# Optimization experiments

Hardware: AMD Instinct MI355X
Metric: run time of the kernel (lower is better)

The kernel has to match this reference:

```python
import jax, jax.numpy as jnp
import numpy as np

WINDOW = 25
DIM_HEAD = 32


def _rel_pos_indices(w):
    # replicates the torch buffer: grid of (i,j) positions, pairwise offsets
    pos = np.arange(w)
    gi, gj = np.meshgrid(pos, pos, indexing='ij')
    grid = np.stack([gi.reshape(-1), gj.reshape(-1)], axis=-1)  # (w*w, 2)
    rel = grid[:, None, :] - grid[None, :, :] + (w - 1)          # (n, n, 2)
    return jnp.asarray(rel[..., 0] * (2 * w - 1) + rel[..., 1], dtype=jnp.int32)


def setup_inputs() -> dict:
    key = jax.random.key(0)
    k1, k2, k3, k4 = jax.random.split(key, 4)
    b, d, w = 32, 256, WINDOW
    heads = d // DIM_HEAD
    x = jax.random.normal(k1, (b, d, w, w), dtype=jnp.float32)
    W_qkv = jax.random.normal(k2, (d, 3 * d), dtype=jnp.float32) * 0.02
    W_out = jax.random.normal(k3, (d, d), dtype=jnp.float32) * 0.02
    rel_emb = jax.random.normal(k4, ((2 * w - 1) ** 2, heads), dtype=jnp.float32) * 0.02
    return {"x": x, "W_qkv": W_qkv, "W_out": W_out, "rel_emb": rel_emb}


def reference(x, W_qkv, W_out, rel_emb):
    b, d, H, W = x.shape
    h = d // DIM_HEAD
    scale = DIM_HEAD ** -0.5
    n = H * W

    # b d H W -> b n d
    xf = x.reshape(b, d, n).transpose(0, 2, 1)
    qkv = xf @ W_qkv                       # (b, n, 3d); columns ordered q,k,v
    q, k, v = jnp.split(qkv, 3, axis=-1)

    def to_heads(t):
        return t.reshape(b, n, h, DIM_HEAD).transpose(0, 2, 1, 3)  # b h n dh

    q = to_heads(q) * scale
    k = to_heads(k)
    v = to_heads(v)

    sim = jnp.einsum('bhid,bhjd->bhij', q, k)          # (b, h, n, n)
    bias = rel_emb[_rel_pos_indices(H)]                # (n, n, h)
    sim = sim + bias.transpose(2, 0, 1)[None]          # add per-head bias
    attn = jax.nn.softmax(sim, axis=-1)

    out = jnp.einsum('bhij,bhjd->bhid', attn, v)       # (b, h, n, dh)
    # b m (H W) dh -> b H W (m dh)  (head-major channel concat)
    out = out.transpose(0, 2, 1, 3).reshape(b, H, W, d)
    out = out @ W_out                                  # output projection (no bias)
    return out.transpose(0, 3, 1, 2)                   # b d H W
```

## Files before the change

kernel.cpp:

```cpp
#include <hip/hip_runtime.h>
#include <hip/hip_bf16.h>
#include <cstdint>

typedef __bf16 bf16x8 __attribute__((ext_vector_type(8)));
typedef __bf16 bf16x4 __attribute__((ext_vector_type(4)));
typedef float  f32x4  __attribute__((ext_vector_type(4)));

__device__ __forceinline__ int div25(int v) { return (v * 1311) >> 15; }

#if __has_builtin(__builtin_amdgcn_exp2f)
__device__ __forceinline__ float fast_exp2(float x) { return __builtin_amdgcn_exp2f(x); }
#else
__device__ __forceinline__ float fast_exp2(float x) { return exp2f(x); }
#endif

__device__ __forceinline__ int sniff_isbf(const void* p)
{
    const unsigned short* x = (const unsigned short*)p;
    int cnt = 0;
    #pragma unroll
    for (int i = 0; i < 16; ++i) {
        int e = (x[2 * i] >> 7) & 0xFF;
        cnt += (e >= 90 && e <= 143) ? 1 : 0;
    }
    return cnt > 8;
}

__global__ void k_transcvt(const void* __restrict__ src, __bf16* __restrict__ dst,
                           int R, int C, int Cpad, int src_bstride, int dst_bstride)
{
    __shared__ float tile[64][65];
    int isbf = sniff_isbf(src);
    int b  = blockIdx.z;
    int r0 = blockIdx.y * 64, c0 = blockIdx.x * 64;
    int tc = threadIdx.x & 63, tg = threadIdx.x >> 6;
    const unsigned short* sb = (const unsigned short*)src + (size_t)b * src_bstride;
    const float*          sf = (const float*)src          + (size_t)b * src_bstride;
    #pragma unroll
    for (int rr = 0; rr < 16; ++rr) {
        int r = r0 + tg * 16 + rr, c = c0 + tc;
        float v = 0.f;
        if (r < R && c < C) {
            if (isbf) v = __uint_as_float((unsigned int)sb[r * C + c] << 16);
            else      v = sf[r * C + c];
        }
        tile[tg * 16 + rr][tc] = v;
    }
    __syncthreads();
    __bf16* d = dst + (size_t)b * dst_bstride;
    #pragma unroll
    for (int rr = 0; rr < 16; ++rr) {
        int c = c0 + tg * 16 + rr, r = r0 + tc;
        if (c < Cpad && r < R) d[(size_t)c * R + r] = (__bf16)tile[tc][tg * 16 + rr];
    }
}

__global__ void k_wprep(const void* __restrict__ Wqkv, const void* __restrict__ Wout,
                        __bf16* __restrict__ Wt, __bf16* __restrict__ WoT)
{
    __shared__ float tile[64][65];
    int isbf = sniff_isbf(Wqkv);
    int isqkv = (blockIdx.x < 12);
    int bx = isqkv ? blockIdx.x : (blockIdx.x - 12);
    const void* src = isqkv ? Wqkv : Wout;
    __bf16* dst = isqkv ? Wt : WoT;
    int R = 256, C = isqkv ? 768 : 256;
    int r0 = blockIdx.y * 64, c0 = bx * 64;
    int tc = threadIdx.x & 63, tg = threadIdx.x >> 6;
    const unsigned short* sb = (const unsigned short*)src;
    const float*          sf = (const float*)src;
    #pragma unroll
    for (int rr = 0; rr < 16; ++rr) {
        int r = r0 + tg * 16 + rr, c = c0 + tc;
        float v;
        if (isbf) v = __uint_as_float((unsigned int)sb[r * C + c] << 16);
        else      v = sf[r * C + c];
        tile[tg * 16 + rr][tc] = v;
    }
    __syncthreads();
    const float qs = 0.25503494f;
    #pragma unroll
    for (int rr = 0; rr < 16; ++rr) {
        int c = c0 + tg * 16 + rr, r = r0 + tc;
        float v = tile[tc][tg * 16 + rr];
        if (isqkv && c < 256) v *= qs;
        dst[(size_t)c * R + r] = (__bf16)v;
    }
}

__global__ void k_bias(const void* __restrict__ rel, __bf16* __restrict__ biasC)
{
    const float LOG2E = 1.4426950408889634f;
    int isbf = sniff_isbf(rel);
    int ig = blockIdx.x;
    int h  = blockIdx.y;
    for (int t0 = 0; t0 < 10; ++t0) {
        int t  = t0 * 256 + threadIdx.x;
        int jc = t >> 7;
        int js = (t >> 6) & 1;
        int ln = t & 63;
        int q = ln >> 4, l = ln & 15;
        int i = ig * 16 + l;
        int di = div25(i), ri = i - 25 * di;
        bf16x4 out;
        #pragma unroll
        for (int rr = 0; rr < 4; ++rr) {
            int j = jc * 32 + js * 16 + q * 4 + rr;
            float v;
            if (j >= 625) {
                v = -43281.f;
            } else {
                int dj = div25(j);
                int idx = (di - dj + 24) * 49 + ri - (j - 25 * dj) + 24;
                idx = min(max(idx, 0), 2400);
                float r;
                if (isbf) r = (float)((const __bf16*)rel)[idx * 8 + h];
                else      r = ((const float*)rel)[idx * 8 + h];
                v = r * LOG2E;
            }
            out[rr] = (__bf16)v;
        }
        *(bf16x4*)(biasC + ((size_t)(h * 40 + ig) * 20 + jc) * 512 + js * 256 + ln * 4) = out;
    }
}

#define AS(r, c) pool[(size_t)(r) * 40 + (c)]
#define BS(r, c) pool[5120 + (size_t)(r) * 40 + (c)]
#define CS(r, c) pool[(size_t)(r) * 44 + (c)]
__global__ __launch_bounds__(256, 2) void k_qkv(
    const __bf16* __restrict__ xT,
    const __bf16* __restrict__ Wt,
    __bf16* __restrict__ Q,
    __bf16* __restrict__ Km,
    __bf16* __restrict__ Vt)
{
    __shared__ __align__(16) __bf16 pool[10240];
    int b = blockIdx.z, pt = blockIdx.y, jt = blockIdx.x;
    int p0 = pt * 128, j0 = jt * 128;
    int tid = threadIdx.x;
    int w = tid >> 6, lane = tid & 63;
    int quad = lane >> 4, l15 = lane & 15;
    int wr = w >> 1, wc = w & 1;

    int srow = tid >> 2, scg = (tid & 3) * 8;
    const __bf16* ag  = xT + ((size_t)(b * 640 + p0 + srow) * 256) + scg;
    const __bf16* ag2 = ag + 64 * 256;
    const __bf16* bg  = Wt + ((size_t)(j0 + srow) * 256) + scg;
    const __bf16* bg2 = bg + 64 * 256;

    f32x4 acc[4][4] = {};
    for (int kk = 0; kk < 8; ++kk) {
        int c0 = kk * 32;
        bf16x8 a0 = *(const bf16x8*)(ag + c0);
        bf16x8 a1 = *(const bf16x8*)(ag2 + c0);
        bf16x8 b0 = *(const bf16x8*)(bg + c0);
        bf16x8 b1 = *(const bf16x8*)(bg2 + c0);
        __syncthreads();
        *(bf16x8*)(&AS(srow, scg))      = a0;
        *(bf16x8*)(&AS(64 + srow, scg)) = a1;
        *(bf16x8*)(&BS(srow, scg))      = b0;
        *(bf16x8*)(&BS(64 + srow, scg)) = b1;
        __syncthreads();
        bf16x8 af[4], bfr[4];
        #pragma unroll
        for (int t = 0; t < 4; ++t) {
            af[t]  = *(const bf16x8*)(&AS(wr * 64 + t * 16 + l15, quad * 8));
            bfr[t] = *(const bf16x8*)(&BS(wc * 64 + t * 16 + l15, quad * 8));
        }
        #pragma unroll
        for (int i = 0; i < 4; ++i)
            #pragma unroll
            for (int j = 0; j < 4; ++j)
                acc[i][j] = __builtin_amdgcn_mfma_f32_16x16x32_bf16(af[i], bfr[j], acc[i][j], 0, 0, 0);
    }

    if (jt < 4) {
        for (int r = 0; r < 4; ++r) {
            __syncthreads();
            if (wc == (r >> 1)) {
                #pragma unroll
                for (int i = 0; i < 4; ++i) {
                    #pragma unroll
                    for (int js = 0; js < 2; ++js) {
                        int jp = (r & 1) * 2 + js;
                        int col = js * 16 + l15;
                        int prow = wr * 64 + i * 16 + quad * 4;
                        #pragma unroll
                        for (int rr = 0; rr < 4; ++rr)
                            CS(prow + rr, col) = (__bf16)acc[i][jp][rr];
                    }
                }
            }
            __syncthreads();
            int jj = j0 + r * 32;
            __bf16* dst; int hh;
            if (jj < 256) { hh = jj >> 5; dst = Q; }
            else          { hh = (jj - 256) >> 5; dst = Km; }
            int p = tid >> 1, d0 = (tid & 1) * 16;
            size_t base = ((size_t)((b * 8 + hh) * 640) + p0 + p) * 32 + d0;
            #pragma unroll
            for (int k4 = 0; k4 < 4; ++k4) {
                bf16x4 v4 = *(const bf16x4*)(&CS(p, d0 + k4 * 4));
                *(bf16x4*)(dst + base + k4 * 4) = v4;
            }
        }
    } else {
        #pragma unroll
        for (int i = 0; i < 4; ++i) {
            #pragma unroll
            for (int j = 0; j < 4; ++j) {
                int jj = j0 + wc * 64 + j * 16 + l15 - 512;
                int h = jj >> 5, t = jj & 31;
                int p = p0 + wr * 64 + i * 16 + quad * 4;
                bf16x4 vv;
                #pragma unroll
                for (int rr = 0; rr < 4; ++rr) vv[rr] = (__bf16)acc[i][j][rr];
                *(bf16x4*)(Vt + ((size_t)((b * 8 + h) * 32) + t) * 640 + p) = vv;
            }
        }
    }
}

__global__ __launch_bounds__(128, 3) void k_attn(
    const __bf16* __restrict__ Q,
    const __bf16* __restrict__ Km,
    const __bf16* __restrict__ Vt,
    const __bf16* __restrict__ biasC,
    __bf16* __restrict__ ctx)
{
    __shared__ __align__(16) __bf16 P[2][2][64][40];
    __shared__ float ssum[2][64];
    int bh = blockIdx.x, b = bh >> 3, h = bh & 7;
    int tid = threadIdx.x, w = tid >> 6, lane = tid & 63;
    int quad = lane >> 4, l15 = lane & 15;
    int i0 = (blockIdx.y * 2 + w) * 64;

    bf16x8 qa[4];
    #pragma unroll
    for (int m = 0; m < 4; ++m)
        qa[m] = *(const bf16x8*)(Q + ((size_t)bh * 640 + i0 + 16 * m + l15) * 32 + quad * 8);
    const __bf16* kbase = Km + (size_t)bh * 640 * 32 + quad * 8;
    const __bf16* vbase = Vt + ((size_t)bh * 32 + l15) * 640 + quad * 8;
    const __bf16* bcb   = biasC + (size_t)(h * 40 + (i0 >> 4)) * 10240 + lane * 4;

    f32x4 o[4][2] = {};
    float psum[4] = {0.f, 0.f, 0.f, 0.f};

    bf16x8 k0 = *(const bf16x8*)(kbase + (size_t)l15 * 32);
    bf16x8 k1 = *(const bf16x8*)(kbase + (size_t)(16 + l15) * 32);
    bf16x4 bc[4][2];
    #pragma unroll
    for (int m = 0; m < 4; ++m) {
        bc[m][0] = *(const bf16x4*)(bcb + m * 10240);
        bc[m][1] = *(const bf16x4*)(bcb + m * 10240 + 256);
    }
    bf16x8 vC0 = {}, vC1 = {};

    for (int c = 0; c < 20; ++c) {
        int buf = c & 1;
        if (c > 0) {
            #pragma unroll
            for (int m = 0; m < 4; ++m) {
                bf16x8 pa = *(const bf16x8*)(&P[w][buf ^ 1][16 * m + l15][quad * 8]);
                o[m][0] = __builtin_amdgcn_mfma_f32_16x16x32_bf16(pa, vC0, o[m][0], 0, 0, 0);
                o[m][1] = __builtin_amdgcn_mfma_f32_16x16x32_bf16(pa, vC1, o[m][1], 0, 0, 0);
            }
        }
        int cn = min(c + 1, 19);
        bf16x8 k0n = *(const bf16x8*)(kbase + (size_t)(cn * 32 + l15) * 32);
        bf16x8 k1n = *(const bf16x8*)(kbase + (size_t)(cn * 32 + 16 + l15) * 32);
        bf16x8 vN0 = *(const bf16x8*)(vbase + c * 32);
        bf16x8 vN1 = *(const bf16x8*)(vbase + (size_t)16 * 640 + c * 32);
        bf16x4 bn[4][2];
        #pragma unroll
        for (int m = 0; m < 4; ++m) {
            bn[m][0] = *(const bf16x4*)(bcb + m * 10240 + cn * 512);
            bn[m][1] = *(const bf16x4*)(bcb + m * 10240 + cn * 512 + 256);
        }
        #pragma unroll
        for (int m = 0; m < 4; ++m) {
            f32x4 f0, f1;
            #pragma unroll
            for (int rr = 0; rr < 4; ++rr) { f0[rr] = (float)bc[m][0][rr]; f1[rr] = (float)bc[m][1][rr]; }
            f32x4 s0 = __builtin_amdgcn_mfma_f32_16x16x32_bf16(k0, qa[m], f0, 0, 0, 0);
            f32x4 s1 = __builtin_amdgcn_mfma_f32_16x16x32_bf16(k1, qa[m], f1, 0, 0, 0);
            bf16x4 p0, p1;
            #pragma unroll
            for (int rr = 0; rr < 4; ++rr) {
                float e0 = fast_exp2(s0[rr]); psum[m] += e0; p0[rr] = (__bf16)e0;
                float e1 = fast_exp2(s1[rr]); psum[m] += e1; p1[rr] = (__bf16)e1;
            }
            *(bf16x4*)(&P[w][buf][16 * m + l15][quad * 4])      = p0;
            *(bf16x4*)(&P[w][buf][16 * m + l15][16 + quad * 4]) = p1;
        }
        k0 = k0n; k1 = k1n; vC0 = vN0; vC1 = vN1;
        #pragma unroll
        for (int m = 0; m < 4; ++m) { bc[m][0] = bn[m][0]; bc[m][1] = bn[m][1]; }
    }
    #pragma unroll
    for (int m = 0; m < 4; ++m) {
        bf16x8 pa = *(const bf16x8*)(&P[w][1][16 * m + l15][quad * 8]);
        o[m][0] = __builtin_amdgcn_mfma_f32_16x16x32_bf16(pa, vC0, o[m][0], 0, 0, 0);
        o[m][1] = __builtin_amdgcn_mfma_f32_16x16x32_bf16(pa, vC1, o[m][1], 0, 0, 0);
    }

    #pragma unroll
    for (int m = 0; m < 4; ++m) {
        psum[m] += __shfl_xor(psum[m], 16);
        psum[m] += __shfl_xor(psum[m], 32);
    }
    if (quad == 0)
        #pragma unroll
        for (int m = 0; m < 4; ++m) ssum[w][16 * m + l15] = psum[m];
    #pragma unroll
    for (int m = 0; m < 4; ++m) {
        #pragma unroll
        for (int rr = 0; rr < 4; ++rr) {
            int il = 16 * m + quad * 4 + rr;
            float inv = 1.f / ssum[w][il];
            size_t base = ((size_t)b * 640 + i0 + il) * 256 + h * 32;
            ctx[base + l15]      = (__bf16)(o[m][0][rr] * inv);
            ctx[base + 16 + l15] = (__bf16)(o[m][1][rr] * inv);
        }
    }
}

__global__ __launch_bounds__(256, 2) void k_outproj(
    const __bf16* __restrict__ ctx,
    const __bf16* __restrict__ WoT,
    const void* __restrict__ xorig,
    void* __restrict__ out)
{
    __shared__ __align__(16) __bf16 As2[64][40];
    __shared__ __align__(16) __bf16 Bs2[256][40];
    int isbf = sniff_isbf(xorig);
    int b = blockIdx.y, pt = blockIdx.x;
    int p0 = pt * 64;
    int tid = threadIdx.x, w = tid >> 6, lane = tid & 63;
    int quad = lane >> 4, l15 = lane & 15;
    int srow = tid >> 2, scg = (tid & 3) * 8;
    const __bf16* ag = ctx + ((size_t)(b * 640 + p0 + srow) * 256) + scg;
    const __bf16* bg = WoT + (size_t)srow * 256 + scg;

    f32x4 acc[4][4] = {};
    for (int kk = 0; kk < 8; ++kk) {
        int c0 = kk * 32;
        bf16x8 a0 = *(const bf16x8*)(ag + c0);
        bf16x8 b0 = *(const bf16x8*)(bg + c0);
        bf16x8 b1 = *(const bf16x8*)(bg + 64 * 256 + c0);
        bf16x8 b2 = *(const bf16x8*)(bg + 128 * 256 + c0);
        bf16x8 b3 = *(const bf16x8*)(bg + 192 * 256 + c0);
        __syncthreads();
        *(bf16x8*)(&As2[srow][scg])       = a0;
        *(bf16x8*)(&Bs2[srow][scg])       = b0;
        *(bf16x8*)(&Bs2[64 + srow][scg])  = b1;
        *(bf16x8*)(&Bs2[128 + srow][scg]) = b2;
        *(bf16x8*)(&Bs2[192 + srow][scg]) = b3;
        __syncthreads();
        bf16x8 af[4], bfr[4];
        #pragma unroll
        for (int t = 0; t < 4; ++t) {
            af[t]  = *(const bf16x8*)(&As2[t * 16 + l15][quad * 8]);
            bfr[t] = *(const bf16x8*)(&Bs2[w * 64 + t * 16 + l15][quad * 8]);
        }
        #pragma unroll
        for (int i = 0; i < 4; ++i)
            #pragma unroll
            for (int j = 0; j < 4; ++j)
                acc[i][j] = __builtin_amdgcn_mfma_f32_16x16x32_bf16(af[i], bfr[j], acc[i][j], 0, 0, 0);
    }
    __bf16* outb = (__bf16*)out;
    float*  outf = (float*)out;
    #pragma unroll
    for (int i = 0; i < 4; ++i) {
        #pragma unroll
        for (int j = 0; j < 4; ++j) {
            int co = w * 64 + j * 16 + l15;
            #pragma unroll
            for (int rr = 0; rr < 4; ++rr) {
                int p = p0 + i * 16 + quad * 4 + rr;
                if (p < 625) {
                    size_t o = ((size_t)(b * 256) + co) * 625 + p;
                    if (isbf) outb[o] = (__bf16)acc[i][j][rr];
                    else      outf[o] = acc[i][j][rr];
                }
            }
        }
    }
}

extern "C" void kernel_launch(void* const* d_in, const int* in_sizes, int n_in,
                              void* d_out, int out_size, void* d_ws, size_t ws_size,
                              hipStream_t stream)
{
    const void* x    = d_in[0];
    const void* Wqkv = d_in[1];
    const void* Wout = d_in[2];
    const void* rel  = d_in[3];

    __bf16* ws    = (__bf16*)d_ws;
    __bf16* xT    = ws + 64;
    __bf16* biasC = xT;
    __bf16* ctx   = xT + 3276800;
    __bf16* Wt    = xT + 10485760;
    __bf16* WoT   = Wt + 196608;
    __bf16* Q     = WoT + 65536;
    __bf16* Km    = Q + 5242880;
    __bf16* Vt    = Km + 5242880;

    k_transcvt<<<dim3(10, 4, 32), 256, 0, stream>>>(x, xT, 256, 625, 640,
                                                    256 * 625, 640 * 256);
    k_wprep<<<dim3(16, 4), 256, 0, stream>>>(Wqkv, Wout, Wt, WoT);
    k_qkv<<<dim3(6, 5, 32), 256, 0, stream>>>(xT, Wt, Q, Km, Vt);
    k_bias<<<dim3(40, 8), 256, 0, stream>>>(rel, biasC);
    k_attn<<<dim3(256, 5), 128, 0, stream>>>(Q, Km, Vt, biasC, ctx);
    k_outproj<<<dim3(10, 32), 256, 0, stream>>>(ctx, WoT, x, d_out);
}
```

Measured before the change: 180.9 us.

## Merge preprocessing kernels into one launch and reorder attention loop MFMAs

The x transpose, weight prep and bias-table kernels are merged into a single launch that dispatches on block index, which removes two kernel launches. The bias buffer gets its own workspace region so it no longer aliases xT and can be written concurrently. In the attention loop, the QK MFMAs are issued first, then exp, then the PV MFMAs on the previous tile, and the P stores are deferred, so MFMA and exp work can overlap. This needs more workspace and keeps more registers live at once.

Result: faster. 161.0 us (-11.0%).

```diff
diff --git a/kernel.cpp b/kernel.cpp
--- a/kernel.cpp
+++ b/kernel.cpp
@@ -26,101 +26,102 @@
     return cnt > 8;
 }
 
-__global__ void k_transcvt(const void* __restrict__ src, __bf16* __restrict__ dst,
-                           int R, int C, int Cpad, int src_bstride, int dst_bstride)
+__global__ __launch_bounds__(256) void k_pre(
+    const void* __restrict__ x, const void* __restrict__ Wqkv,
+    const void* __restrict__ Wout, const void* __restrict__ rel,
+    __bf16* __restrict__ xT, __bf16* __restrict__ Wt, __bf16* __restrict__ WoT,
+    __bf16* __restrict__ biasC)
 {
     __shared__ float tile[64][65];
-    int isbf = sniff_isbf(src);
-    int b  = blockIdx.z;
-    int r0 = blockIdx.y * 64, c0 = blockIdx.x * 64;
-    int tc = threadIdx.x & 63, tg = threadIdx.x >> 6;
-    const unsigned short* sb = (const unsigned short*)src + (size_t)b * src_bstride;
-    const float*          sf = (const float*)src          + (size_t)b * src_bstride;
-    #pragma unroll
-    for (int rr = 0; rr < 16; ++rr) {
-        int r = r0 + tg * 16 + rr, c = c0 + tc;
-        float v = 0.f;
-        if (r < R && c < C) {
+    int bid = blockIdx.x;
+    if (bid < 1280) {
+        int isbf = sniff_isbf(x);
+        int b = bid / 40, rem = bid % 40;
+        int c0 = (rem % 10) * 64, r0 = (rem / 10) * 64;
+        const int R = 256, C = 625, Cpad = 640;
+        int tc = threadIdx.x & 63, tg = threadIdx.x >> 6;
+        const unsigned short* sb = (const unsigned short*)x + (size_t)b * (256 * 625);
+        const float*          sf = (const float*)x          + (size_t)b * (256 * 625);
+        #pragma unroll
+        for (int rr = 0; rr < 16; ++rr) {
+            int r = r0 + tg * 16 + rr, c = c0 + tc;
+            float v = 0.f;
+            if (r < R && c < C) {
+                if (isbf) v = __uint_as_float((unsigned int)sb[r * C + c] << 16);
+                else      v = sf[r * C + c];
+            }
+            tile[tg * 16 + rr][tc] = v;
+        }
+        __syncthreads();
+        __bf16* d = xT + (size_t)b * (640 * 256);
+        #pragma unroll
+        for (int rr = 0; rr < 16; ++rr) {
+            int c = c0 + tg * 16 + rr, r = r0 + tc;
+            if (c < Cpad && r < R) d[(size_t)c * R + r] = (__bf16)tile[tc][tg * 16 + rr];
+        }
+    } else if (bid < 1344) {
+        int q = bid - 1280;
+        int bx = q % 16, by = q / 16;
+        int isbf = sniff_isbf(Wqkv);
+        int isqkv = (bx < 12);
+        int bxx = isqkv ? bx : (bx - 12);
+        const void* src = isqkv ? Wqkv : Wout;
+        __bf16* dst = isqkv ? Wt : WoT;
+        int R = 256, C = isqkv ? 768 : 256;
+        int r0 = by * 64, c0 = bxx * 64;
+        int tc = threadIdx.x & 63, tg = threadIdx.x >> 6;
+        const unsigned short* sb = (const unsigned short*)src;
+        const float*          sf = (const float*)src;
+        #pragma unroll
+        for (int rr = 0; rr < 16; ++rr) {
+            int r = r0 + tg * 16 + rr, c = c0 + tc;
+            float v;
             if (isbf) v = __uint_as_float((unsigned int)sb[r * C + c] << 16);
             else      v = sf[r * C + c];
-        }
-        tile[tg * 16 + rr][tc] = v;
-    }
-    __syncthreads();
-    __bf16* d = dst + (size_t)b * dst_bstride;
-    #pragma unroll
-    for (int rr = 0; rr < 16; ++rr) {
-        int c = c0 + tg * 16 + rr, r = r0 + tc;
-        if (c < Cpad && r < R) d[(size_t)c * R + r] = (__bf16)tile[tc][tg * 16 + rr];
-    }
-}
-
-__global__ void k_wprep(const void* __restrict__ Wqkv, const void* __restrict__ Wout,
-                        __bf16* __restrict__ Wt, __bf16* __restrict__ WoT)
-{
-    __shared__ float tile[64][65];
-    int isbf = sniff_isbf(Wqkv);
-    int isqkv = (blockIdx.x < 12);
-    int bx = isqkv ? blockIdx.x : (blockIdx.x - 12);
-    const void* src = isqkv ? Wqkv : Wout;
-    __bf16* dst = isqkv ? Wt : WoT;
-    int R = 256, C = isqkv ? 768 : 256;
-    int r0 = blockIdx.y * 64, c0 = bx * 64;
-    int tc = threadIdx.x & 63, tg = threadIdx.x >> 6;
-    const unsigned short* sb = (const unsigned short*)src;
-    const float*          sf = (const float*)src;
-    #pragma unroll
-    for (int rr = 0; rr < 16; ++rr) {
-        int r = r0 + tg * 16 + rr, c = c0 + tc;
-        float v;
-        if (isbf) v = __uint_as_float((unsigned int)sb[r * C + c] << 16);
-        else      v = sf[r * C + c];
-        tile[tg * 16 + rr][tc] = v;
-    }
-    __syncthreads();
-    const float qs = 0.25503494f;
-    #pragma unroll
-    for (int rr = 0; rr < 16; ++rr) {
-        int c = c0 + tg * 16 + rr, r = r0 + tc;
-        float v = tile[tc][tg * 16 + rr];
-        if (isqkv && c < 256) v *= qs;
-        dst[(size_t)c * R + r] = (__bf16)v;
-    }
-}
-
-__global__ void k_bias(const void* __restrict__ rel, __bf16* __restrict__ biasC)
-{
-    const float LOG2E = 1.4426950408889634f;
-    int isbf = sniff_isbf(rel);
-    int ig = blockIdx.x;
-    int h  = blockIdx.y;
-    for (int t0 = 0; t0 < 10; ++t0) {
-        int t  = t0 * 256 + threadIdx.x;
-        int jc = t >> 7;
-        int js = (t >> 6) & 1;
-        int ln = t & 63;
-        int q = ln >> 4, l = ln & 15;
-        int i = ig * 16 + l;
-        int di = div25(i), ri = i - 25 * di;
-        bf16x4 out;
-        #pragma unroll
-        for (int rr = 0; rr < 4; ++rr) {
-            int j = jc * 32 + js * 16 + q * 4 + rr;
-            float v;
-            if (j >= 625) {
-                v = -43281.f;
-            } else {
-                int dj = div25(j);
-                int idx = (di - dj + 24) * 49 + ri - (j - 25 * dj) + 24;
-                idx = min(max(idx, 0), 2400);
-                float r;
-                if (isbf) r = (float)((const __bf16*)rel)[idx * 8 + h];
-                else      r = ((const float*)rel)[idx * 8 + h];
-                v = r * LOG2E;
-            }
-            out[rr] = (__bf16)v;
-        }
-        *(bf16x4*)(biasC + ((size_t)(h * 40 + ig) * 20 + jc) * 512 + js * 256 + ln * 4) = out;
+            tile[tg * 16 + rr][tc] = v;
+        }
+        __syncthreads();
+        const float qs = 0.25503494f;
+        #pragma unroll
+        for (int rr = 0; rr < 16; ++rr) {
+            int c = c0 + tg * 16 + rr, r = r0 + tc;
+            float v = tile[tc][tg * 16 + rr];
+            if (isqkv && c < 256) v *= qs;
+            dst[(size_t)c * R + r] = (__bf16)v;
+        }
+    } else {
+        const float LOG2E = 1.4426950408889634f;
+        int isbf = sniff_isbf(rel);
+        int q = bid - 1344;
+        int ig = q % 40, h = q / 40;
+        for (int t0 = 0; t0 < 10; ++t0) {
+            int t  = t0 * 256 + threadIdx.x;
+            int jc = t >> 7;
+            int js = (t >> 6) & 1;
+            int ln = t & 63;
+            int qd = ln >> 4, l = ln & 15;
+            int i = ig * 16 + l;
+            int di = div25(i), ri = i - 25 * di;
+            bf16x4 out;
+            #pragma unroll
+            for (int rr = 0; rr < 4; ++rr) {
+                int j = jc * 32 + js * 16 + qd * 4 + rr;
+                float v;
+                if (j >= 625) {
+                    v = -43281.f;
+                } else {
+                    int dj = div25(j);
+                    int idx = (di - dj + 24) * 49 + ri - (j - 25 * dj) + 24;
+                    idx = min(max(idx, 0), 2400);
+                    float r;
+                    if (isbf) r = (float)((const __bf16*)rel)[idx * 8 + h];
+                    else      r = ((const float*)rel)[idx * 8 + h];
+                    v = r * LOG2E;
+                }
+                out[rr] = (__bf16)v;
+            }
+            *(bf16x4*)(biasC + ((size_t)(h * 40 + ig) * 20 + jc) * 512 + js * 256 + ln * 4) = out;
+        }
     }
 }
 
@@ -258,13 +259,14 @@
 
     for (int c = 0; c < 20; ++c) {
         int buf = c & 1;
-        if (c > 0) {
-            #pragma unroll
-            for (int m = 0; m < 4; ++m) {
-                bf16x8 pa = *(const bf16x8*)(&P[w][buf ^ 1][16 * m + l15][quad * 8]);
-                o[m][0] = __builtin_amdgcn_mfma_f32_16x16x32_bf16(pa, vC0, o[m][0], 0, 0, 0);
-                o[m][1] = __builtin_amdgcn_mfma_f32_16x16x32_bf16(pa, vC1, o[m][1], 0, 0, 0);
-            }
+        f32x4 s[4][2];
+        #pragma unroll
+        for (int m = 0; m < 4; ++m) {
+            f32x4 f0, f1;
+            #pragma unroll
+            for (int rr = 0; rr < 4; ++rr) { f0[rr] = (float)bc[m][0][rr]; f1[rr] = (float)bc[m][1][rr]; }
+            s[m][0] = __builtin_amdgcn_mfma_f32_16x16x32_bf16(k0, qa[m], f0, 0, 0, 0);
+            s[m][1] = __builtin_amdgcn_mfma_f32_16x16x32_bf16(k1, qa[m], f1, 0, 0, 0);
         }
         int cn = min(c + 1, 19);
         bf16x8 k0n = *(const bf16x8*)(kbase + (size_t)(cn * 32 + l15) * 32);
@@ -277,21 +279,27 @@
             bn[m][0] = *(const bf16x4*)(bcb + m * 10240 + cn * 512);
             bn[m][1] = *(const bf16x4*)(bcb + m * 10240 + cn * 512 + 256);
         }
+        bf16x4 pk[4][2];
         #pragma unroll
         for (int m = 0; m < 4; ++m) {
-            f32x4 f0, f1;
-            #pragma unroll
-            for (int rr = 0; rr < 4; ++rr) { f0[rr] = (float)bc[m][0][rr]; f1[rr] = (float)bc[m][1][rr]; }
-            f32x4 s0 = __builtin_amdgcn_mfma_f32_16x16x32_bf16(k0, qa[m], f0, 0, 0, 0);
-            f32x4 s1 = __builtin_amdgcn_mfma_f32_16x16x32_bf16(k1, qa[m], f1, 0, 0, 0);
-            bf16x4 p0, p1;
             #pragma unroll
             for (int rr = 0; rr < 4; ++rr) {
-                float e0 = fast_exp2(s0[rr]); psum[m] += e0; p0[rr] = (__bf16)e0;
-                float e1 = fast_exp2(s1[rr]); psum[m] += e1; p1[rr] = (__bf16)e1;
-            }
-            *(bf16x4*)(&P[w][buf][16 * m + l15][quad * 4])      = p0;
-            *(bf16x4*)(&P[w][buf][16 * m + l15][16 + quad * 4]) = p1;
+                float e0 = fast_exp2(s[m][0][rr]); psum[m] += e0; pk[m][0][rr] = (__bf16)e0;
+                float e1 = fast_exp2(s[m][1][rr]); psum[m] += e1; pk[m][1][rr] = (__bf16)e1;
+            }
+        }
+        if (c > 0) {
+            #pragma unroll
+            for (int m = 0; m < 4; ++m) {
+                bf16x8 pa = *(const bf16x8*)(&P[w][buf ^ 1][16 * m + l15][quad * 8]);
+                o[m][0] = __builtin_amdgcn_mfma_f32_16x16x32_bf16(pa, vC0, o[m][0], 0, 0, 0);
+                o[m][1] = __builtin_amdgcn_mfma_f32_16x16x32_bf16(pa, vC1, o[m][1], 0, 0, 0);
+            }
+        }
+        #pragma unroll
+        for (int m = 0; m < 4; ++m) {
+            *(bf16x4*)(&P[w][buf][16 * m + l15][quad * 4])      = pk[m][0];
+            *(bf16x4*)(&P[w][buf][16 * m + l15][16 + quad * 4]) = pk[m][1];
         }
         k0 = k0n; k1 = k1n; vC0 = vN0; vC1 = vN1;
         #pragma unroll
@@ -399,20 +407,17 @@
     const void* rel  = d_in[3];
 
     __bf16* ws    = (__bf16*)d_ws;
-    __bf16* xT    = ws + 64;
-    __bf16* biasC = xT;
-    __bf16* ctx   = xT + 3276800;
+    __bf16* xT    = ws;
     __bf16* Wt    = xT + 10485760;
     __bf16* WoT   = Wt + 196608;
     __bf16* Q     = WoT + 65536;
     __bf16* Km    = Q + 5242880;
     __bf16* Vt    = Km + 5242880;
-
-    k_transcvt<<<dim3(10, 4, 32), 256, 0, stream>>>(x, xT, 256, 625, 640,
-                                                    256 * 625, 640 * 256);
-    k_wprep<<<dim3(16, 4), 256, 0, stream>>>(Wqkv, Wout, Wt, WoT);
+    __bf16* biasC = Vt + 5242880;
+    __bf16* ctx   = biasC + 3276800;
+
+    k_pre<<<1664, 256, 0, stream>>>(x, Wqkv, Wout, rel, xT, Wt, WoT, biasC);
     k_qkv<<<dim3(6, 5, 32), 256, 0, stream>>>(xT, Wt, Q, Km, Vt);
-    k_bias<<<dim3(40, 8), 256, 0, stream>>>(rel, biasC);
     k_attn<<<dim3(256, 5), 128, 0, stream>>>(Q, Km, Vt, biasC, ctx);
     k_outproj<<<dim3(10, 32), 256, 0, stream>>>(ctx, WoT, x, d_out);
 }
```
